# Performance work log

Measured on AMD Instinct MI355X. Metric: run time of the kernel, lower is better.

## Reference

```python
import jax, jax.numpy as jnp
import numpy as np

NUM_CODES = 1024
CODE_DIM = 256
EMA_DECAY = 0.99
COMMITMENT = 0.25
EPS = 1e-6


def setup_inputs() -> dict:
    key = jax.random.key(0)
    k1, k2 = jax.random.split(key)
    z = jax.random.normal(k1, (64, 512, CODE_DIM), dtype=jnp.float32)
    embedding = jax.random.normal(k2, (NUM_CODES, CODE_DIM), dtype=jnp.float32)
    cluster_size = jnp.zeros((NUM_CODES,), dtype=jnp.float32)
    embedding_avg = embedding.copy()
    return {"z": z, "embedding": embedding, "cluster_size": cluster_size,
            "embedding_avg": embedding_avg}


def reference(z, embedding, cluster_size, embedding_avg):
    K, D = embedding.shape
    flat = z.reshape(-1, D)                                  # [N, D]
    dist = (jnp.sum(flat * flat, axis=1, keepdims=True)
            - 2.0 * (flat @ embedding.T)
            + jnp.sum(embedding * embedding, axis=1))
    indices = jnp.argmin(dist, axis=1)                       # [N]
    z_q = embedding[indices].reshape(z.shape)

    # EMA codebook update (training branch, no-grad in original)
    counts = jax.ops.segment_sum(jnp.ones_like(indices, dtype=flat.dtype),
                                 indices, num_segments=K)    # one-hot col sums
    embed_sum = jax.ops.segment_sum(flat, indices, num_segments=K)  # [K, D]
    new_cluster_size = cluster_size * EMA_DECAY + (1.0 - EMA_DECAY) * counts
    new_embedding_avg = embedding_avg * EMA_DECAY + (1.0 - EMA_DECAY) * embed_sum
    n = jnp.sum(new_cluster_size)
    cs = (new_cluster_size + EPS) / (n + K * EPS)
    new_embedding = new_embedding_avg / cs[:, None]

    loss = COMMITMENT * jnp.mean((jax.lax.stop_gradient(z_q) - z) ** 2)
    z_q_st = z + jax.lax.stop_gradient(z_q - z)
    return (z_q_st, loss, indices, new_cluster_size, new_embedding_avg,
            new_embedding)
```

## Files before the change

kernel.cpp:

```cpp
#include <hip/hip_runtime.h>

#define N_ROWS   32768
#define KCODES   1024
#define DDIM     256
#define RPB      64
#define NBLK     512

#define O_ZQ     0
#define O_LOSS   8388608
#define O_IDX    8388609
#define O_NCS    8421377
#define O_NEA    8422401
#define O_NEMB   8684545

#define W_ESUM   0
#define W_CNT    262144
#define W_ENORM  263168
#define W_LOSSP  264192
#define W_N      265728
#define W_IDX    265792
#define W_SORT   298560
#define W_RANK   331328

typedef _Float16 half_t;
typedef __attribute__((ext_vector_type(8))) _Float16 half8;
typedef __attribute__((ext_vector_type(4))) float floatx4;

__global__ __launch_bounds__(256)
void k_prep2(const float* __restrict__ emb, float* __restrict__ enorm,
             half_t* __restrict__ Bp, float* __restrict__ zero_ws) {
    __shared__ half_t hi[16 * 256];
    __shared__ half_t lo[16 * 256];
    __shared__ float  ssum[256];
    const int ct  = blockIdx.x;
    const int tid = threadIdx.x;
    const int c16 = tid >> 4;
    const int dp  = tid & 15;

    {
        float4 z4 = {0.f, 0.f, 0.f, 0.f};
        float4* wsf4 = (float4*)zero_ws;
        int t = ct * 256 + tid;
        #pragma unroll
        for (int i = 0; i < 4; ++i) wsf4[t + i * 16384] = z4;
        if (t < 256) wsf4[65536 + t] = z4;
    }

    float ss = 0.f;
    #pragma unroll
    for (int i = 0; i < 4; ++i) {
        float4 v = *(const float4*)(emb + (size_t)(ct * 16 + c16) * DDIM + dp * 16 + i * 4);
        ss += v.x * v.x + v.y * v.y + v.z * v.z + v.w * v.w;
        #pragma unroll
        for (int q = 0; q < 4; ++q) {
            float f = (&v.x)[q];
            half_t h = (half_t)f;
            hi[c16 * 256 + dp * 16 + i * 4 + q] = h;
            lo[c16 * 256 + dp * 16 + i * 4 + q] = (half_t)(f - (float)h);
        }
    }
    ssum[tid] = ss;
    __syncthreads();
    if (tid < 16) {
        float s = 0.f;
        #pragma unroll
        for (int i = 0; i < 16; ++i) s += ssum[tid * 16 + i];
        enorm[ct * 16 + tid] = s;
    }

    const int g16 = ((ct >> 4) << 2) | ((ct >> 2) & 3);
    const int ns  = ct & 3;
    #pragma unroll
    for (int i = 0; i < 4; ++i) {
        int f    = tid + i * 256;
        int ks   = f >> 6;
        int lane = f & 63;
        int cc   = lane & 15;
        int seg  = ks >> 3;
        int ko   = (ks & 7) * 32 + (lane >> 4) * 8;
        const half_t* src = (seg == 1) ? lo : hi;
        half8 v = *(const half8*)(src + cc * 256 + ko);
        *(half8*)(Bp + (((size_t)(g16 * 16 + ks) * 4 + ns) * 64 + lane) * 8) = v;
    }
}

__global__ __launch_bounds__(512)
void k_argmin(const float* __restrict__ z, const half_t* __restrict__ Bp,
              const float* __restrict__ enorm, const float* __restrict__ embf,
              int* __restrict__ out_idx, float* __restrict__ out_idx_f,
              float* __restrict__ out_zq, float* __restrict__ lossp,
              int* __restrict__ counts_i, int* __restrict__ rank_ws) {
    __shared__ __align__(16) half_t As[RPB * 512];

    const int tid  = threadIdx.x;
    const int w    = tid >> 6;
    const int lane = tid & 63;
    const int tx   = lane & 15;
    const int quad = lane >> 4;
    const int rh   = w >> 2;
    const int cq   = w & 3;
    const int rbase = blockIdx.x * RPB;

    {
        const int arow = w * 8 + (lane >> 3);
        const int sw   = arow & 7;
        #pragma unroll
        for (int it = 0; it < 4; ++it) {
            int g = it * 8 + (lane & 7);
            const float* zp = z + (size_t)(rbase + arow) * DDIM + g * 8;
            float4 v0 = *(const float4*)zp;
            float4 v1 = *(const float4*)(zp + 4);
            half8 hi, lo;
            hi[0] = (half_t)v0.x; lo[0] = (half_t)(v0.x - (float)hi[0]);
            hi[1] = (half_t)v0.y; lo[1] = (half_t)(v0.y - (float)hi[1]);
            hi[2] = (half_t)v0.z; lo[2] = (half_t)(v0.z - (float)hi[2]);
            hi[3] = (half_t)v0.w; lo[3] = (half_t)(v0.w - (float)hi[3]);
            hi[4] = (half_t)v1.x; lo[4] = (half_t)(v1.x - (float)hi[4]);
            hi[5] = (half_t)v1.y; lo[5] = (half_t)(v1.y - (float)hi[5]);
            hi[6] = (half_t)v1.z; lo[6] = (half_t)(v1.z - (float)hi[6]);
            hi[7] = (half_t)v1.w; lo[7] = (half_t)(v1.w - (float)hi[7]);
            *(half8*)(&As[arow * 512 + ((g ^ sw)) * 8])        = hi;
            *(half8*)(&As[arow * 512 + (((32 + g) ^ sw)) * 8]) = lo;
        }
    }
    __syncthreads();

    floatx4 zero4 = {0.f, 0.f, 0.f, 0.f};
    float bd[2][4];
    int   bi[2][4];
    #pragma unroll
    for (int mt = 0; mt < 2; ++mt)
        #pragma unroll
        for (int r = 0; r < 4; ++r) { bd[mt][r] = 3.402823466e38f; bi[mt][r] = 0; }

    for (int g4 = 0; g4 < 4; ++g4) {
        const int cb = cq * 256 + g4 * 64;
        const half_t* Bg = Bp + (size_t)(cq * 4 + g4) * 32768 + (size_t)lane * 8;

        floatx4 acc[2][4];
        #pragma unroll
        for (int mt = 0; mt < 2; ++mt)
            #pragma unroll
            for (int ns = 0; ns < 4; ++ns) acc[mt][ns] = zero4;

        half8 B0[4], B1[4];
        #define LOADB(PK, BUF)                                                 \
            { const half_t* bp_ = Bg + (PK) * 2048;                            \
              _Pragma("unroll")                                                \
              for (int ns = 0; ns < 4; ++ns)                                   \
                  BUF[ns] = *(const half8*)(bp_ + ns * 512); }
        #define MFMA_BLK(AF, BUF)                                              \
            _Pragma("unroll")                                                  \
            for (int mt = 0; mt < 2; ++mt)                                     \
                _Pragma("unroll")                                              \
                for (int ns = 0; ns < 4; ++ns)                                 \
                    acc[mt][ns] = __builtin_amdgcn_mfma_f32_16x16x32_f16(      \
                        AF[mt], BUF[ns], acc[mt][ns], 0, 0, 0);

        LOADB(0, B0);
        LOADB(1, B1);

        #pragma unroll 2
        for (int s = 0; s < 8; ++s) {
            half8 a0[2], a1[2];
            #pragma unroll
            for (int mt = 0; mt < 2; ++mt) {
                int row = rh * 32 + mt * 16 + tx;
                int sw  = row & 7;
                a0[mt] = *(half8*)(&As[row * 512 + ((s * 4 + quad) ^ sw) * 8]);
                a1[mt] = *(half8*)(&As[row * 512 + ((32 + s * 4 + quad) ^ sw) * 8]);
            }
            if (s & 1) { MFMA_BLK(a0, B1) MFMA_BLK(a1, B1) LOADB(s + 2, B1); }
            else       { MFMA_BLK(a0, B0) MFMA_BLK(a1, B0) LOADB(s + 2, B0); }
        }
        #pragma unroll 2
        for (int s = 8; s < 16; ++s) {
            half8 a0[2];
            #pragma unroll
            for (int mt = 0; mt < 2; ++mt) {
                int row = rh * 32 + mt * 16 + tx;
                int sw  = row & 7;
                a0[mt] = *(half8*)(&As[row * 512 + (((s - 8) * 4 + quad) ^ sw) * 8]);
            }
            if (s & 1) { MFMA_BLK(a0, B1) if (s + 2 < 16) LOADB(s + 2, B1); }
            else       { MFMA_BLK(a0, B0) if (s + 2 < 16) LOADB(s + 2, B0); }
        }
        #undef LOADB
        #undef MFMA_BLK

        #pragma unroll
        for (int ns = 0; ns < 4; ++ns) {
            float en = enorm[cb + ns * 16 + tx];
            int   cc = cb + ns * 16 + tx;
            #pragma unroll
            for (int mt = 0; mt < 2; ++mt)
                #pragma unroll
                for (int r = 0; r < 4; ++r) {
                    float d = fmaf(-2.f, acc[mt][ns][r], en);
                    if (d < bd[mt][r]) { bd[mt][r] = d; bi[mt][r] = cc; }
                }
        }
    }

    #pragma unroll
    for (int mt = 0; mt < 2; ++mt)
        #pragma unroll
        for (int r = 0; r < 4; ++r) {
            float d = bd[mt][r];
            int   b = bi[mt][r];
            #pragma unroll
            for (int off = 8; off > 0; off >>= 1) {
                float od = __shfl_xor(d, off);
                int   ob = __shfl_xor(b, off);
                if (od < d || (od == d && ob < b)) { d = od; b = ob; }
            }
            bd[mt][r] = d; bi[mt][r] = b;
        }

    __syncthreads();
    float* sd   = (float*)As;
    int*   si   = ((int*)As) + 256;
    int*   sidx = ((int*)As) + 512;
    if (tx == 0) {
        #pragma unroll
        for (int mt = 0; mt < 2; ++mt)
            #pragma unroll
            for (int r = 0; r < 4; ++r) {
                int row = rh * 32 + mt * 16 + quad * 4 + r;
                sd[row * 4 + cq] = bd[mt][r];
                si[row * 4 + cq] = bi[mt][r];
            }
    }
    __syncthreads();
    if (tid < RPB) {
        int row = tid;
        float d = sd[row * 4];
        int   b = si[row * 4];
        #pragma unroll
        for (int ww = 1; ww < 4; ++ww) {
            float od = sd[row * 4 + ww];
            int   ob = si[row * 4 + ww];
            if (od < d || (od == d && ob < b)) { d = od; b = ob; }
        }
        sidx[row] = b;
        out_idx[rbase + row]   = b;
        out_idx_f[rbase + row] = (float)b;
        int rk = atomicAdd(&counts_i[b], 1);
        rank_ws[rbase + row] = rk;
    }
    __syncthreads();

    float l = 0.f;
    #pragma unroll
    for (int u = 0; u < 8; ++u) {
        int gi  = tid + u * 512;
        int row = gi >> 6;
        int c4  = gi & 63;
        int k   = sidx[row];
        float4 zv = *(const float4*)(z    + (size_t)(rbase + row) * DDIM + c4 * 4);
        float4 ev = *(const float4*)(embf + (size_t)k * DDIM + c4 * 4);
        float dx = ev.x - zv.x, dy = ev.y - zv.y, dz = ev.z - zv.z, dw = ev.w - zv.w;
        float4 o = { zv.x + dx, zv.y + dy, zv.z + dz, zv.w + dw };
        *(float4*)(out_zq + (size_t)(rbase + row) * DDIM + c4 * 4) = o;
        l += dx * dx + dy * dy + dz * dz + dw * dw;
    }
    #pragma unroll
    for (int off = 32; off > 0; off >>= 1) l += __shfl_down(l, off);
    __shared__ float ls[8];
    if (lane == 0) ls[w] = l;
    __syncthreads();
    if (tid == 0) {
        float s = 0.f;
        #pragma unroll
        for (int i = 0; i < 8; ++i) s += ls[i];
        lossp[blockIdx.x] = s;
    }
}

__global__ __launch_bounds__(256)
void k_scatter(const float* __restrict__ cs_in, const int* __restrict__ counts_i,
               const float* __restrict__ lossp, const int* __restrict__ idx,
               const int* __restrict__ rank_ws, int* __restrict__ rows_sorted,
               float* __restrict__ out_ncs, float* __restrict__ n_ws,
               float* __restrict__ loss_out) {
    const int tid = threadIdx.x;
    const int bid = blockIdx.x;
    __shared__ int ps[256];
    __shared__ int base_s[1024];
    __shared__ float sv[4], sl[4];

    int c[4]; int pt = 0;
    #pragma unroll
    for (int i = 0; i < 4; ++i) { c[i] = counts_i[tid * 4 + i]; pt += c[i]; }
    ps[tid] = pt;
    __syncthreads();
    for (int s = 1; s < 256; s <<= 1) {
        int v = (tid >= s) ? ps[tid - s] : 0;
        __syncthreads();
        ps[tid] += v;
        __syncthreads();
    }
    int o = ps[tid] - pt;
    float v = 0.f;
    #pragma unroll
    for (int i = 0; i < 4; ++i) {
        base_s[tid * 4 + i] = o;
        o += c[i];
        if (bid == 0) {
            float nc = cs_in[tid * 4 + i] * 0.99f + 0.01f * (float)c[i];
            out_ncs[tid * 4 + i] = nc;
            v += nc;
        }
    }
    if (bid == 0) {
        float l = lossp[tid] + lossp[tid + 256];
        #pragma unroll
        for (int off = 32; off > 0; off >>= 1) {
            v += __shfl_down(v, off);
            l += __shfl_down(l, off);
        }
        if ((tid & 63) == 0) { sv[tid >> 6] = v; sl[tid >> 6] = l; }
    }
    __syncthreads();
    if (bid == 0 && tid == 0) {
        n_ws[0]     = sv[0] + sv[1] + sv[2] + sv[3];
        loss_out[0] = 0.25f * ((sl[0] + sl[1] + sl[2] + sl[3]) / 8388608.0f);
    }
    int r = bid * 256 + tid;
    int k = idx[r];
    rows_sorted[base_s[k] + rank_ws[r]] = r;
}

__global__ __launch_bounds__(256)
void k_esum2(const float* __restrict__ z, const int* __restrict__ rows_sorted,
             const int* __restrict__ idx, float* __restrict__ esum) {
    const int tid  = threadIdx.x;
    const int w    = tid >> 6;
    const int lane = tid & 63;
    const int base = (blockIdx.x * 4 + w) * 32;

    int r = rows_sorted[base + (lane & 31)];
    int c = idx[r];
    float4 acc = {0.f, 0.f, 0.f, 0.f};
    #pragma unroll 8
    for (int j = 0; j < 32; ++j) {
        int rj = __shfl(r, j);
        int cj = __shfl(c, j);
        float4 zv = *(const float4*)(z + (size_t)rj * DDIM + lane * 4);
        acc.x += zv.x; acc.y += zv.y; acc.z += zv.z; acc.w += zv.w;
        int cn = (j < 31) ? __shfl(c, j + 1) : -1;
        if (cn != cj) {
            float* p = esum + (size_t)cj * DDIM + lane * 4;
            atomicAdd(p + 0, acc.x);
            atomicAdd(p + 1, acc.y);
            atomicAdd(p + 2, acc.z);
            atomicAdd(p + 3, acc.w);
            acc.x = 0.f; acc.y = 0.f; acc.z = 0.f; acc.w = 0.f;
        }
    }
}

__global__ __launch_bounds__(256)
void k_embed(const float* __restrict__ ea, const float* __restrict__ esum,
             const float* __restrict__ ncs, const float* __restrict__ n_ws,
             float* __restrict__ out_nea, float* __restrict__ out_nemb) {
    const int tid = threadIdx.x;
    const int kb  = blockIdx.x * 4;
    const int c   = tid >> 6;
    const int l   = tid & 63;
    size_t off = (size_t)(kb + c) * DDIM + l * 4;
    float4 av = *(const float4*)(ea   + off);
    float4 ev = *(const float4*)(esum + off);
    float4 nea = { av.x * 0.99f + 0.01f * ev.x,
                   av.y * 0.99f + 0.01f * ev.y,
                   av.z * 0.99f + 0.01f * ev.z,
                   av.w * 0.99f + 0.01f * ev.w };
    *(float4*)(out_nea + off) = nea;
    float csv = (ncs[kb + c] + 1e-6f) / (n_ws[0] + 0.001024f);
    float4 nemb = { nea.x / csv, nea.y / csv, nea.z / csv, nea.w / csv };
    *(float4*)(out_nemb + off) = nemb;
}

extern "C" void kernel_launch(void* const* d_in, const int* in_sizes, int n_in,
                              void* d_out, int out_size, void* d_ws, size_t ws_size,
                              hipStream_t stream) {
    const float* z   = (const float*)d_in[0];
    const float* emb = (const float*)d_in[1];
    const float* cs  = (const float*)d_in[2];
    const float* ea  = (const float*)d_in[3];
    float* out = (float*)d_out;
    float* ws  = (float*)d_ws;

    float* esum    = ws + W_ESUM;
    int*   cnts    = (int*)(ws + W_CNT);
    float* enorm   = ws + W_ENORM;
    float* lossp   = ws + W_LOSSP;
    float* wn      = ws + W_N;
    int*   widx    = (int*)(ws + W_IDX);
    int*   rsorted = (int*)(ws + W_SORT);
    int*   rankw   = (int*)(ws + W_RANK);

    half_t* Bp = (half_t*)(out + O_NEA + 3);

    k_prep2   <<<64, 256, 0, stream>>>(emb, enorm, Bp, ws);
    k_argmin  <<<NBLK, 512, 0, stream>>>(z, Bp, enorm, emb,
                                         widx, out + O_IDX, out + O_ZQ, lossp,
                                         cnts, rankw);
    k_scatter <<<128, 256, 0, stream>>>(cs, cnts, lossp, widx, rankw, rsorted,
                                        out + O_NCS, wn, out + O_LOSS);
    k_esum2   <<<256, 256, 0, stream>>>(z, rsorted, widx, esum);
    k_embed   <<<256, 256, 0, stream>>>(ea, esum, out + O_NCS, wn,
                                        out + O_NEA, out + O_NEMB);
}
```

Before: 179.8 us.

## Fuse scatter, esum and embed kernels into one with grid-wide spin barriers

Merges the three tail kernels into one persistent 256-block kernel. Two software grid barriers built from atomic counters in workspace replace the launch boundaries between them. Each block recomputes the cluster-size total locally, so it no longer goes through workspace. The aim is to remove two kernel launch gaps; the cost is spin-wait overhead and reliance on all 256 blocks being resident at once to avoid deadlock.

```diff
diff --git a/kernel.cpp b/kernel.cpp
--- a/kernel.cpp
+++ b/kernel.cpp
@@ -17,7 +17,7 @@
 #define W_CNT    262144
 #define W_ENORM  263168
 #define W_LOSSP  264192
-#define W_N      265728
+#define W_BAR    264704
 #define W_IDX    265792
 #define W_SORT   298560
 #define W_RANK   331328
@@ -44,6 +44,10 @@
         #pragma unroll
         for (int i = 0; i < 4; ++i) wsf4[t + i * 16384] = z4;
         if (t < 256) wsf4[65536 + t] = z4;
+        if (t == 0) {
+            int* b = (int*)(zero_ws + W_BAR);
+            b[0] = 0; b[1] = 0;
+        }
     }
 
     float ss = 0.f;
@@ -277,14 +281,29 @@
     }
 }
 
+__device__ __forceinline__ void grid_spin(int* bar, int expected) {
+    __syncthreads();
+    __threadfence();
+    if (threadIdx.x == 0) {
+        atomicAdd(bar, 1);
+        while (atomicAdd(bar, 0) < expected) __builtin_amdgcn_s_sleep(8);
+    }
+    __syncthreads();
+    __threadfence();
+}
+
 __global__ __launch_bounds__(256)
-void k_scatter(const float* __restrict__ cs_in, const int* __restrict__ counts_i,
-               const float* __restrict__ lossp, const int* __restrict__ idx,
-               const int* __restrict__ rank_ws, int* __restrict__ rows_sorted,
-               float* __restrict__ out_ncs, float* __restrict__ n_ws,
-               float* __restrict__ loss_out) {
-    const int tid = threadIdx.x;
-    const int bid = blockIdx.x;
+void k_tail3(const float* __restrict__ cs_in, const int* __restrict__ counts_i,
+             const float* __restrict__ lossp, const int* __restrict__ idx,
+             const int* __restrict__ rank_ws, const float* __restrict__ z,
+             const float* __restrict__ ea, int* __restrict__ rows_sorted,
+             float* __restrict__ esum, int* __restrict__ bar,
+             float* __restrict__ out_ncs, float* __restrict__ loss_out,
+             float* __restrict__ out_nea, float* __restrict__ out_nemb) {
+    const int tid  = threadIdx.x;
+    const int bid  = blockIdx.x;
+    const int w    = tid >> 6;
+    const int lane = tid & 63;
     __shared__ int ps[256];
     __shared__ int base_s[1024];
     __shared__ float sv[4], sl[4];
@@ -301,84 +320,76 @@
         __syncthreads();
     }
     int o = ps[tid] - pt;
-    float v = 0.f;
+    float pn = 0.f;
     #pragma unroll
     for (int i = 0; i < 4; ++i) {
         base_s[tid * 4 + i] = o;
         o += c[i];
-        if (bid == 0) {
-            float nc = cs_in[tid * 4 + i] * 0.99f + 0.01f * (float)c[i];
-            out_ncs[tid * 4 + i] = nc;
-            v += nc;
-        }
-    }
-    if (bid == 0) {
-        float l = lossp[tid] + lossp[tid + 256];
-        #pragma unroll
-        for (int off = 32; off > 0; off >>= 1) {
-            v += __shfl_down(v, off);
-            l += __shfl_down(l, off);
-        }
-        if ((tid & 63) == 0) { sv[tid >> 6] = v; sl[tid >> 6] = l; }
-    }
-    __syncthreads();
-    if (bid == 0 && tid == 0) {
-        n_ws[0]     = sv[0] + sv[1] + sv[2] + sv[3];
+        float nc = cs_in[tid * 4 + i] * 0.99f + 0.01f * (float)c[i];
+        pn += nc;
+        if (bid == 0) out_ncs[tid * 4 + i] = nc;
+    }
+    float pl = (bid == 0) ? (lossp[tid] + lossp[tid + 256]) : 0.f;
+    #pragma unroll
+    for (int off = 32; off > 0; off >>= 1) {
+        pn += __shfl_down(pn, off);
+        pl += __shfl_down(pl, off);
+    }
+    if (lane == 0) { sv[w] = pn; sl[w] = pl; }
+    __syncthreads();
+    const float nval = sv[0] + sv[1] + sv[2] + sv[3];
+    if (bid == 0 && tid == 0)
         loss_out[0] = 0.25f * ((sl[0] + sl[1] + sl[2] + sl[3]) / 8388608.0f);
-    }
-    int r = bid * 256 + tid;
-    int k = idx[r];
-    rows_sorted[base_s[k] + rank_ws[r]] = r;
-}
-
-__global__ __launch_bounds__(256)
-void k_esum2(const float* __restrict__ z, const int* __restrict__ rows_sorted,
-             const int* __restrict__ idx, float* __restrict__ esum) {
-    const int tid  = threadIdx.x;
-    const int w    = tid >> 6;
-    const int lane = tid & 63;
-    const int base = (blockIdx.x * 4 + w) * 32;
-
-    int r = rows_sorted[base + (lane & 31)];
-    int c = idx[r];
-    float4 acc = {0.f, 0.f, 0.f, 0.f};
-    #pragma unroll 8
-    for (int j = 0; j < 32; ++j) {
-        int rj = __shfl(r, j);
-        int cj = __shfl(c, j);
-        float4 zv = *(const float4*)(z + (size_t)rj * DDIM + lane * 4);
-        acc.x += zv.x; acc.y += zv.y; acc.z += zv.z; acc.w += zv.w;
-        int cn = (j < 31) ? __shfl(c, j + 1) : -1;
-        if (cn != cj) {
-            float* p = esum + (size_t)cj * DDIM + lane * 4;
-            atomicAdd(p + 0, acc.x);
-            atomicAdd(p + 1, acc.y);
-            atomicAdd(p + 2, acc.z);
-            atomicAdd(p + 3, acc.w);
-            acc.x = 0.f; acc.y = 0.f; acc.z = 0.f; acc.w = 0.f;
-        }
-    }
-}
-
-__global__ __launch_bounds__(256)
-void k_embed(const float* __restrict__ ea, const float* __restrict__ esum,
-             const float* __restrict__ ncs, const float* __restrict__ n_ws,
-             float* __restrict__ out_nea, float* __restrict__ out_nemb) {
-    const int tid = threadIdx.x;
-    const int kb  = blockIdx.x * 4;
-    const int c   = tid >> 6;
-    const int l   = tid & 63;
-    size_t off = (size_t)(kb + c) * DDIM + l * 4;
-    float4 av = *(const float4*)(ea   + off);
-    float4 ev = *(const float4*)(esum + off);
-    float4 nea = { av.x * 0.99f + 0.01f * ev.x,
-                   av.y * 0.99f + 0.01f * ev.y,
-                   av.z * 0.99f + 0.01f * ev.z,
-                   av.w * 0.99f + 0.01f * ev.w };
-    *(float4*)(out_nea + off) = nea;
-    float csv = (ncs[kb + c] + 1e-6f) / (n_ws[0] + 0.001024f);
-    float4 nemb = { nea.x / csv, nea.y / csv, nea.z / csv, nea.w / csv };
-    *(float4*)(out_nemb + off) = nemb;
+    if (tid < 128) {
+        int r = bid * 128 + tid;
+        int k = idx[r];
+        atomicExch(&rows_sorted[base_s[k] + rank_ws[r]], r);
+    }
+
+    grid_spin(&bar[0], 256);
+
+    {
+        const int base = (bid * 4 + w) * 32;
+        int r = rows_sorted[base + (lane & 31)];
+        int cc = idx[r];
+        float4 acc = {0.f, 0.f, 0.f, 0.f};
+        #pragma unroll 8
+        for (int j = 0; j < 32; ++j) {
+            int rj = __shfl(r, j);
+            int cj = __shfl(cc, j);
+            float4 zv = *(const float4*)(z + (size_t)rj * DDIM + lane * 4);
+            acc.x += zv.x; acc.y += zv.y; acc.z += zv.z; acc.w += zv.w;
+            int cn = (j < 31) ? __shfl(cc, j + 1) : -1;
+            if (cn != cj) {
+                float* p = esum + (size_t)cj * DDIM + lane * 4;
+                atomicAdd(p + 0, acc.x);
+                atomicAdd(p + 1, acc.y);
+                atomicAdd(p + 2, acc.z);
+                atomicAdd(p + 3, acc.w);
+                acc.x = 0.f; acc.y = 0.f; acc.z = 0.f; acc.w = 0.f;
+            }
+        }
+    }
+
+    grid_spin(&bar[1], 256);
+
+    {
+        const int kb = bid * 4;
+        const int cc = tid >> 6;
+        const int l  = tid & 63;
+        size_t off = (size_t)(kb + cc) * DDIM + l * 4;
+        float4 av = *(const float4*)(ea   + off);
+        float4 ev = *(const float4*)(esum + off);
+        float4 nea = { av.x * 0.99f + 0.01f * ev.x,
+                       av.y * 0.99f + 0.01f * ev.y,
+                       av.z * 0.99f + 0.01f * ev.z,
+                       av.w * 0.99f + 0.01f * ev.w };
+        *(float4*)(out_nea + off) = nea;
+        float ncv = cs_in[kb + cc] * 0.99f + 0.01f * (float)counts_i[kb + cc];
+        float csv = (ncv + 1e-6f) / (nval + 0.001024f);
+        float4 nemb = { nea.x / csv, nea.y / csv, nea.z / csv, nea.w / csv };
+        *(float4*)(out_nemb + off) = nemb;
+    }
 }
 
 extern "C" void kernel_launch(void* const* d_in, const int* in_sizes, int n_in,
@@ -395,20 +406,19 @@
     int*   cnts    = (int*)(ws + W_CNT);
     float* enorm   = ws + W_ENORM;
     float* lossp   = ws + W_LOSSP;
-    float* wn      = ws + W_N;
+    int*   bar     = (int*)(ws + W_BAR);
     int*   widx    = (int*)(ws + W_IDX);
     int*   rsorted = (int*)(ws + W_SORT);
     int*   rankw   = (int*)(ws + W_RANK);
 
     half_t* Bp = (half_t*)(out + O_NEA + 3);
 
-    k_prep2   <<<64, 256, 0, stream>>>(emb, enorm, Bp, ws);
-    k_argmin  <<<NBLK, 512, 0, stream>>>(z, Bp, enorm, emb,
-                                         widx, out + O_IDX, out + O_ZQ, lossp,
-                                         cnts, rankw);
-    k_scatter <<<128, 256, 0, stream>>>(cs, cnts, lossp, widx, rankw, rsorted,
-                                        out + O_NCS, wn, out + O_LOSS);
-    k_esum2   <<<256, 256, 0, stream>>>(z, rsorted, widx, esum);
-    k_embed   <<<256, 256, 0, stream>>>(ea, esum, out + O_NCS, wn,
-                                        out + O_NEA, out + O_NEMB);
+    k_prep2  <<<64, 256, 0, stream>>>(emb, enorm, Bp, ws);
+    k_argmin <<<NBLK, 512, 0, stream>>>(z, Bp, enorm, emb,
+                                        widx, out + O_IDX, out + O_ZQ, lossp,
+                                        cnts, rankw);
+    k_tail3  <<<256, 256, 0, stream>>>(cs, cnts, lossp, widx, rankw, z, ea,
+                                       rsorted, esum, bar,
+                                       out + O_NCS, out + O_LOSS,
+                                       out + O_NEA, out + O_NEMB);
 }
```

Measured after the change: 260.9 us. 1.45x slower.

## Fuse EMA embedding update into esum via per-code completion counters; retile argmin waves

Applied to the files above, without the earlier changes.

The separate k_embed launch is removed. Each code's new embedding_avg and embedding are now written by whichever wave finishes the last segment of that code, detected with an atomic per-code row counter. Empty codes are handled in k_scatter, which now computes n redundantly in every block. The argmin MFMA wave mapping also changes: each wave now covers all 64 rows and 32 codes per pass instead of 32 rows by 64 codes, so it loads fewer B fragments and more A fragments from LDS. The cost is a full vmcnt wait after each atomic flush plus extra atomic traffic, in exchange for one fewer kernel launch and one fewer pass over esum.

```diff
diff --git a/kernel.cpp b/kernel.cpp
--- a/kernel.cpp
+++ b/kernel.cpp
@@ -15,8 +15,9 @@
 
 #define W_ESUM   0
 #define W_CNT    262144
-#define W_ENORM  263168
-#define W_LOSSP  264192
+#define W_DONE   263168
+#define W_ENORM  264192
+#define W_LOSSP  265216
 #define W_N      265728
 #define W_IDX    265792
 #define W_SORT   298560
@@ -43,7 +44,7 @@
         int t = ct * 256 + tid;
         #pragma unroll
         for (int i = 0; i < 4; ++i) wsf4[t + i * 16384] = z4;
-        if (t < 256) wsf4[65536 + t] = z4;
+        if (t < 512) wsf4[65536 + t] = z4;
     }
 
     float ss = 0.f;
@@ -97,8 +98,6 @@
     const int lane = tid & 63;
     const int tx   = lane & 15;
     const int quad = lane >> 4;
-    const int rh   = w >> 2;
-    const int cq   = w & 3;
     const int rbase = blockIdx.x * RPB;
 
     {
@@ -126,74 +125,73 @@
     __syncthreads();
 
     floatx4 zero4 = {0.f, 0.f, 0.f, 0.f};
-    float bd[2][4];
-    int   bi[2][4];
-    #pragma unroll
-    for (int mt = 0; mt < 2; ++mt)
+    float bd[4][4];
+    int   bi[4][4];
+    #pragma unroll
+    for (int mt = 0; mt < 4; ++mt)
         #pragma unroll
         for (int r = 0; r < 4; ++r) { bd[mt][r] = 3.402823466e38f; bi[mt][r] = 0; }
 
-    for (int g4 = 0; g4 < 4; ++g4) {
-        const int cb = cq * 256 + g4 * 64;
-        const half_t* Bg = Bp + (size_t)(cq * 4 + g4) * 32768 + (size_t)lane * 8;
-
-        floatx4 acc[2][4];
-        #pragma unroll
-        for (int mt = 0; mt < 2; ++mt)
+    for (int g = 0; g < 4; ++g) {
+        const int slot = 2 * w + (g >> 1);
+        const int ns0  = (g & 1) * 2;
+        const int cb   = (slot >> 2) * 256 + (slot & 3) * 64 + ns0 * 16;
+        const half_t* Bg = Bp + (size_t)slot * 32768 + ns0 * 512 + (size_t)lane * 8;
+
+        floatx4 acc[4][2];
+        #pragma unroll
+        for (int mt = 0; mt < 4; ++mt)
             #pragma unroll
-            for (int ns = 0; ns < 4; ++ns) acc[mt][ns] = zero4;
-
-        half8 B0[4], B1[4];
+            for (int ns = 0; ns < 2; ++ns) acc[mt][ns] = zero4;
+
+        half8 B0[2], B1[2];
         #define LOADB(PK, BUF)                                                 \
             { const half_t* bp_ = Bg + (PK) * 2048;                            \
-              _Pragma("unroll")                                                \
-              for (int ns = 0; ns < 4; ++ns)                                   \
-                  BUF[ns] = *(const half8*)(bp_ + ns * 512); }
-        #define MFMA_BLK(AF, BUF)                                              \
+              BUF[0] = *(const half8*)(bp_);                                   \
+              BUF[1] = *(const half8*)(bp_ + 512); }
+        #define LDA(K8)                                                        \
             _Pragma("unroll")                                                  \
-            for (int mt = 0; mt < 2; ++mt)                                     \
+            for (int mt = 0; mt < 4; ++mt) {                                   \
+                int row = mt * 16 + tx;                                        \
+                a[mt] = *(half8*)(&As[row * 512 + (((K8) + quad) ^ (row & 7)) * 8]); \
+            }
+        #define MFMA_BLK(BUF)                                                  \
+            _Pragma("unroll")                                                  \
+            for (int mt = 0; mt < 4; ++mt)                                     \
                 _Pragma("unroll")                                              \
-                for (int ns = 0; ns < 4; ++ns)                                 \
+                for (int ns = 0; ns < 2; ++ns)                                 \
                     acc[mt][ns] = __builtin_amdgcn_mfma_f32_16x16x32_f16(      \
-                        AF[mt], BUF[ns], acc[mt][ns], 0, 0, 0);
+                        a[mt], BUF[ns], acc[mt][ns], 0, 0, 0);
 
         LOADB(0, B0);
         LOADB(1, B1);
 
         #pragma unroll 2
         for (int s = 0; s < 8; ++s) {
-            half8 a0[2], a1[2];
-            #pragma unroll
-            for (int mt = 0; mt < 2; ++mt) {
-                int row = rh * 32 + mt * 16 + tx;
-                int sw  = row & 7;
-                a0[mt] = *(half8*)(&As[row * 512 + ((s * 4 + quad) ^ sw) * 8]);
-                a1[mt] = *(half8*)(&As[row * 512 + ((32 + s * 4 + quad) ^ sw) * 8]);
-            }
-            if (s & 1) { MFMA_BLK(a0, B1) MFMA_BLK(a1, B1) LOADB(s + 2, B1); }
-            else       { MFMA_BLK(a0, B0) MFMA_BLK(a1, B0) LOADB(s + 2, B0); }
+            half8 a[4];
+            LDA(s * 4)
+            if (s & 1) { MFMA_BLK(B1) } else { MFMA_BLK(B0) }
+            LDA(32 + s * 4)
+            if (s & 1) { MFMA_BLK(B1) LOADB(s + 2, B1); }
+            else       { MFMA_BLK(B0) LOADB(s + 2, B0); }
         }
         #pragma unroll 2
         for (int s = 8; s < 16; ++s) {
-            half8 a0[2];
-            #pragma unroll
-            for (int mt = 0; mt < 2; ++mt) {
-                int row = rh * 32 + mt * 16 + tx;
-                int sw  = row & 7;
-                a0[mt] = *(half8*)(&As[row * 512 + (((s - 8) * 4 + quad) ^ sw) * 8]);
-            }
-            if (s & 1) { MFMA_BLK(a0, B1) if (s + 2 < 16) LOADB(s + 2, B1); }
-            else       { MFMA_BLK(a0, B0) if (s + 2 < 16) LOADB(s + 2, B0); }
+            half8 a[4];
+            LDA((s - 8) * 4)
+            if (s & 1) { MFMA_BLK(B1) if (s + 2 < 16) LOADB(s + 2, B1); }
+            else       { MFMA_BLK(B0) if (s + 2 < 16) LOADB(s + 2, B0); }
         }
         #undef LOADB
+        #undef LDA
         #undef MFMA_BLK
 
         #pragma unroll
-        for (int ns = 0; ns < 4; ++ns) {
+        for (int ns = 0; ns < 2; ++ns) {
             float en = enorm[cb + ns * 16 + tx];
             int   cc = cb + ns * 16 + tx;
             #pragma unroll
-            for (int mt = 0; mt < 2; ++mt)
+            for (int mt = 0; mt < 4; ++mt)
                 #pragma unroll
                 for (int r = 0; r < 4; ++r) {
                     float d = fmaf(-2.f, acc[mt][ns][r], en);
@@ -203,7 +201,7 @@
     }
 
     #pragma unroll
-    for (int mt = 0; mt < 2; ++mt)
+    for (int mt = 0; mt < 4; ++mt)
         #pragma unroll
         for (int r = 0; r < 4; ++r) {
             float d = bd[mt][r];
@@ -219,27 +217,27 @@
 
     __syncthreads();
     float* sd   = (float*)As;
-    int*   si   = ((int*)As) + 256;
-    int*   sidx = ((int*)As) + 512;
+    int*   si   = ((int*)As) + 512;
+    int*   sidx = ((int*)As) + 1024;
     if (tx == 0) {
         #pragma unroll
-        for (int mt = 0; mt < 2; ++mt)
+        for (int mt = 0; mt < 4; ++mt)
             #pragma unroll
             for (int r = 0; r < 4; ++r) {
-                int row = rh * 32 + mt * 16 + quad * 4 + r;
-                sd[row * 4 + cq] = bd[mt][r];
-                si[row * 4 + cq] = bi[mt][r];
+                int row = mt * 16 + quad * 4 + r;
+                sd[row * 8 + w] = bd[mt][r];
+                si[row * 8 + w] = bi[mt][r];
             }
     }
     __syncthreads();
     if (tid < RPB) {
         int row = tid;
-        float d = sd[row * 4];
-        int   b = si[row * 4];
-        #pragma unroll
-        for (int ww = 1; ww < 4; ++ww) {
-            float od = sd[row * 4 + ww];
-            int   ob = si[row * 4 + ww];
+        float d = sd[row * 8];
+        int   b = si[row * 8];
+        #pragma unroll
+        for (int ww = 1; ww < 8; ++ww) {
+            float od = sd[row * 8 + ww];
+            int   ob = si[row * 8 + ww];
             if (od < d || (od == d && ob < b)) { d = od; b = ob; }
         }
         sidx[row] = b;
@@ -280,11 +278,15 @@
 __global__ __launch_bounds__(256)
 void k_scatter(const float* __restrict__ cs_in, const int* __restrict__ counts_i,
                const float* __restrict__ lossp, const int* __restrict__ idx,
-               const int* __restrict__ rank_ws, int* __restrict__ rows_sorted,
+               const int* __restrict__ rank_ws, const float* __restrict__ ea,
+               int* __restrict__ rows_sorted,
                float* __restrict__ out_ncs, float* __restrict__ n_ws,
-               float* __restrict__ loss_out) {
+               float* __restrict__ loss_out,
+               float* __restrict__ out_nea, float* __restrict__ out_nemb) {
     const int tid = threadIdx.x;
     const int bid = blockIdx.x;
+    const int w    = tid >> 6;
+    const int lane = tid & 63;
     __shared__ int ps[256];
     __shared__ int base_s[1024];
     __shared__ float sv[4], sl[4];
@@ -301,53 +303,74 @@
         __syncthreads();
     }
     int o = ps[tid] - pt;
-    float v = 0.f;
+    float pn = 0.f;
     #pragma unroll
     for (int i = 0; i < 4; ++i) {
         base_s[tid * 4 + i] = o;
         o += c[i];
-        if (bid == 0) {
-            float nc = cs_in[tid * 4 + i] * 0.99f + 0.01f * (float)c[i];
-            out_ncs[tid * 4 + i] = nc;
-            v += nc;
-        }
-    }
-    if (bid == 0) {
-        float l = lossp[tid] + lossp[tid + 256];
-        #pragma unroll
-        for (int off = 32; off > 0; off >>= 1) {
-            v += __shfl_down(v, off);
-            l += __shfl_down(l, off);
-        }
-        if ((tid & 63) == 0) { sv[tid >> 6] = v; sl[tid >> 6] = l; }
-    }
-    __syncthreads();
+        float nc = cs_in[tid * 4 + i] * 0.99f + 0.01f * (float)c[i];
+        pn += nc;
+        if (bid == 0) out_ncs[tid * 4 + i] = nc;
+    }
+    float pl = (bid == 0) ? (lossp[tid] + lossp[tid + 256]) : 0.f;
+    #pragma unroll
+    for (int off = 32; off > 0; off >>= 1) {
+        pn += __shfl_down(pn, off);
+        pl += __shfl_down(pl, off);
+    }
+    if (lane == 0) { sv[w] = pn; sl[w] = pl; }
+    __syncthreads();
+    const float nval = sv[0] + sv[1] + sv[2] + sv[3];
     if (bid == 0 && tid == 0) {
-        n_ws[0]     = sv[0] + sv[1] + sv[2] + sv[3];
+        n_ws[0]     = nval;
         loss_out[0] = 0.25f * ((sl[0] + sl[1] + sl[2] + sl[3]) / 8388608.0f);
     }
-    int r = bid * 256 + tid;
-    int k = idx[r];
-    rows_sorted[base_s[k] + rank_ws[r]] = r;
+    {
+        int r = bid * 256 + tid;
+        int k = idx[r];
+        rows_sorted[base_s[k] + rank_ws[r]] = r;
+    }
+    #pragma unroll
+    for (int pass = 0; pass < 2; ++pass) {
+        int k = bid * 8 + pass * 4 + (tid >> 6);
+        if (counts_i[k] == 0) {
+            int l2 = tid & 63;
+            size_t off = (size_t)k * DDIM + l2 * 4;
+            float4 av = *(const float4*)(ea + off);
+            float4 nea = { av.x * 0.99f, av.y * 0.99f, av.z * 0.99f, av.w * 0.99f };
+            *(float4*)(out_nea + off) = nea;
+            float ncv = cs_in[k] * 0.99f;
+            float csv = (ncv + 1e-6f) / (nval + 0.001024f);
+            float4 nemb = { nea.x / csv, nea.y / csv, nea.z / csv, nea.w / csv };
+            *(float4*)(out_nemb + off) = nemb;
+        }
+    }
 }
 
 __global__ __launch_bounds__(256)
-void k_esum2(const float* __restrict__ z, const int* __restrict__ rows_sorted,
-             const int* __restrict__ idx, float* __restrict__ esum) {
+void k_esum3(const float* __restrict__ z, const int* __restrict__ rows_sorted,
+             const int* __restrict__ idx, const int* __restrict__ counts_i,
+             const float* __restrict__ cs_in, const float* __restrict__ n_ws,
+             const float* __restrict__ ea, float* __restrict__ esum,
+             int* __restrict__ done,
+             float* __restrict__ out_nea, float* __restrict__ out_nemb) {
     const int tid  = threadIdx.x;
     const int w    = tid >> 6;
     const int lane = tid & 63;
     const int base = (blockIdx.x * 4 + w) * 32;
+    const float nval = n_ws[0];
 
     int r = rows_sorted[base + (lane & 31)];
     int c = idx[r];
     float4 acc = {0.f, 0.f, 0.f, 0.f};
-    #pragma unroll 8
+    int rlen = 0;
+    #pragma unroll 4
     for (int j = 0; j < 32; ++j) {
         int rj = __shfl(r, j);
         int cj = __shfl(c, j);
         float4 zv = *(const float4*)(z + (size_t)rj * DDIM + lane * 4);
         acc.x += zv.x; acc.y += zv.y; acc.z += zv.z; acc.w += zv.w;
+        rlen++;
         int cn = (j < 31) ? __shfl(c, j + 1) : -1;
         if (cn != cj) {
             float* p = esum + (size_t)cj * DDIM + lane * 4;
@@ -355,30 +378,36 @@
             atomicAdd(p + 1, acc.y);
             atomicAdd(p + 2, acc.z);
             atomicAdd(p + 3, acc.w);
+            asm volatile("s_waitcnt vmcnt(0)" ::: "memory");
+            int last = 0;
+            if (lane == 0) {
+                int old = atomicAdd(&done[cj], rlen);
+                last = (old + rlen == counts_i[cj]) ? 1 : 0;
+            }
+            last = __shfl(last, 0);
+            if (last) {
+                float* q = esum + (size_t)cj * DDIM + lane * 4;
+                float4 ev;
+                ev.x = atomicAdd(q + 0, 0.f);
+                ev.y = atomicAdd(q + 1, 0.f);
+                ev.z = atomicAdd(q + 2, 0.f);
+                ev.w = atomicAdd(q + 3, 0.f);
+                size_t off = (size_t)cj * DDIM + lane * 4;
+                float4 av = *(const float4*)(ea + off);
+                float4 nea = { av.x * 0.99f + 0.01f * ev.x,
+                               av.y * 0.99f + 0.01f * ev.y,
+                               av.z * 0.99f + 0.01f * ev.z,
+                               av.w * 0.99f + 0.01f * ev.w };
+                *(float4*)(out_nea + off) = nea;
+                float ncv = cs_in[cj] * 0.99f + 0.01f * (float)counts_i[cj];
+                float csv = (ncv + 1e-6f) / (nval + 0.001024f);
+                float4 nemb = { nea.x / csv, nea.y / csv, nea.z / csv, nea.w / csv };
+                *(float4*)(out_nemb + off) = nemb;
+            }
             acc.x = 0.f; acc.y = 0.f; acc.z = 0.f; acc.w = 0.f;
-        }
-    }
-}
-
-__global__ __launch_bounds__(256)
-void k_embed(const float* __restrict__ ea, const float* __restrict__ esum,
-             const float* __restrict__ ncs, const float* __restrict__ n_ws,
-             float* __restrict__ out_nea, float* __restrict__ out_nemb) {
-    const int tid = threadIdx.x;
-    const int kb  = blockIdx.x * 4;
-    const int c   = tid >> 6;
-    const int l   = tid & 63;
-    size_t off = (size_t)(kb + c) * DDIM + l * 4;
-    float4 av = *(const float4*)(ea   + off);
-    float4 ev = *(const float4*)(esum + off);
-    float4 nea = { av.x * 0.99f + 0.01f * ev.x,
-                   av.y * 0.99f + 0.01f * ev.y,
-                   av.z * 0.99f + 0.01f * ev.z,
-                   av.w * 0.99f + 0.01f * ev.w };
-    *(float4*)(out_nea + off) = nea;
-    float csv = (ncs[kb + c] + 1e-6f) / (n_ws[0] + 0.001024f);
-    float4 nemb = { nea.x / csv, nea.y / csv, nea.z / csv, nea.w / csv };
-    *(float4*)(out_nemb + off) = nemb;
+            rlen = 0;
+        }
+    }
 }
 
 extern "C" void kernel_launch(void* const* d_in, const int* in_sizes, int n_in,
@@ -393,6 +422,7 @@
 
     float* esum    = ws + W_ESUM;
     int*   cnts    = (int*)(ws + W_CNT);
+    int*   done    = (int*)(ws + W_DONE);
     float* enorm   = ws + W_ENORM;
     float* lossp   = ws + W_LOSSP;
     float* wn      = ws + W_N;
@@ -406,9 +436,9 @@
     k_argmin  <<<NBLK, 512, 0, stream>>>(z, Bp, enorm, emb,
                                          widx, out + O_IDX, out + O_ZQ, lossp,
                                          cnts, rankw);
-    k_scatter <<<128, 256, 0, stream>>>(cs, cnts, lossp, widx, rankw, rsorted,
-                                        out + O_NCS, wn, out + O_LOSS);
-    k_esum2   <<<256, 256, 0, stream>>>(z, rsorted, widx, esum);
-    k_embed   <<<256, 256, 0, stream>>>(ea, esum, out + O_NCS, wn,
+    k_scatter <<<128, 256, 0, stream>>>(cs, cnts, lossp, widx, rankw, ea,
+                                        rsorted, out + O_NCS, wn, out + O_LOSS,
                                         out + O_NEA, out + O_NEMB);
+    k_esum3   <<<256, 256, 0, stream>>>(z, rsorted, widx, cnts, cs, wn, ea,
+                                        esum, done, out + O_NEA, out + O_NEMB);
 }
```

After: 184.3 us. 1.03x slower.

## Halve rows per block and split codebook across all eight waves

Applied to the files above, without the earlier changes.

Each argmin block now handles 32 rows instead of 64, so twice as many blocks launch. All eight waves share the same 32 rows, and each wave scans 128 codes instead of 256. The cross-wave reduction now combines eight candidates per row, and the finalize kernel sums 1024 loss partials. This is meant to improve occupancy and load balance across CUs, at the cost of doubling total codebook reads from L2 and giving each B fragment less reuse.

```diff
diff --git a/kernel.cpp b/kernel.cpp
--- a/kernel.cpp
+++ b/kernel.cpp
@@ -3,8 +3,8 @@
 #define N_ROWS   32768
 #define KCODES   1024
 #define DDIM     256
-#define RPB      64
-#define NBLK     512
+#define RPB      32
+#define NBLK     1024
 
 #define O_ZQ     0
 #define O_LOSS   8388608
@@ -97,31 +97,28 @@
     const int lane = tid & 63;
     const int tx   = lane & 15;
     const int quad = lane >> 4;
-    const int rh   = w >> 2;
-    const int cq   = w & 3;
     const int rbase = blockIdx.x * RPB;
 
-    {
-        const int arow = w * 8 + (lane >> 3);
-        const int sw   = arow & 7;
-        #pragma unroll
-        for (int it = 0; it < 4; ++it) {
-            int g = it * 8 + (lane & 7);
-            const float* zp = z + (size_t)(rbase + arow) * DDIM + g * 8;
-            float4 v0 = *(const float4*)zp;
-            float4 v1 = *(const float4*)(zp + 4);
-            half8 hi, lo;
-            hi[0] = (half_t)v0.x; lo[0] = (half_t)(v0.x - (float)hi[0]);
-            hi[1] = (half_t)v0.y; lo[1] = (half_t)(v0.y - (float)hi[1]);
-            hi[2] = (half_t)v0.z; lo[2] = (half_t)(v0.z - (float)hi[2]);
-            hi[3] = (half_t)v0.w; lo[3] = (half_t)(v0.w - (float)hi[3]);
-            hi[4] = (half_t)v1.x; lo[4] = (half_t)(v1.x - (float)hi[4]);
-            hi[5] = (half_t)v1.y; lo[5] = (half_t)(v1.y - (float)hi[5]);
-            hi[6] = (half_t)v1.z; lo[6] = (half_t)(v1.z - (float)hi[6]);
-            hi[7] = (half_t)v1.w; lo[7] = (half_t)(v1.w - (float)hi[7]);
-            *(half8*)(&As[arow * 512 + ((g ^ sw)) * 8])        = hi;
-            *(half8*)(&As[arow * 512 + (((32 + g) ^ sw)) * 8]) = lo;
-        }
+    #pragma unroll
+    for (int it = 0; it < 2; ++it) {
+        int f   = tid + it * 512;
+        int row = f >> 5;
+        int g   = f & 31;
+        const float* zp = z + (size_t)(rbase + row) * DDIM + g * 8;
+        float4 v0 = *(const float4*)zp;
+        float4 v1 = *(const float4*)(zp + 4);
+        half8 hi, lo;
+        hi[0] = (half_t)v0.x; lo[0] = (half_t)(v0.x - (float)hi[0]);
+        hi[1] = (half_t)v0.y; lo[1] = (half_t)(v0.y - (float)hi[1]);
+        hi[2] = (half_t)v0.z; lo[2] = (half_t)(v0.z - (float)hi[2]);
+        hi[3] = (half_t)v0.w; lo[3] = (half_t)(v0.w - (float)hi[3]);
+        hi[4] = (half_t)v1.x; lo[4] = (half_t)(v1.x - (float)hi[4]);
+        hi[5] = (half_t)v1.y; lo[5] = (half_t)(v1.y - (float)hi[5]);
+        hi[6] = (half_t)v1.z; lo[6] = (half_t)(v1.z - (float)hi[6]);
+        hi[7] = (half_t)v1.w; lo[7] = (half_t)(v1.w - (float)hi[7]);
+        int sw = row & 7;
+        *(half8*)(&As[row * 512 + ((g ^ sw)) * 8])        = hi;
+        *(half8*)(&As[row * 512 + (((32 + g) ^ sw)) * 8]) = lo;
     }
     __syncthreads();
 
@@ -133,9 +130,10 @@
         #pragma unroll
         for (int r = 0; r < 4; ++r) { bd[mt][r] = 3.402823466e38f; bi[mt][r] = 0; }
 
-    for (int g4 = 0; g4 < 4; ++g4) {
-        const int cb = cq * 256 + g4 * 64;
-        const half_t* Bg = Bp + (size_t)(cq * 4 + g4) * 32768 + (size_t)lane * 8;
+    for (int gs = 0; gs < 2; ++gs) {
+        const int slot = 2 * w + gs;
+        const int cb   = slot * 64;
+        const half_t* Bg = Bp + (size_t)slot * 32768 + (size_t)lane * 8;
 
         floatx4 acc[2][4];
         #pragma unroll
@@ -165,7 +163,7 @@
             half8 a0[2], a1[2];
             #pragma unroll
             for (int mt = 0; mt < 2; ++mt) {
-                int row = rh * 32 + mt * 16 + tx;
+                int row = mt * 16 + tx;
                 int sw  = row & 7;
                 a0[mt] = *(half8*)(&As[row * 512 + ((s * 4 + quad) ^ sw) * 8]);
                 a1[mt] = *(half8*)(&As[row * 512 + ((32 + s * 4 + quad) ^ sw) * 8]);
@@ -178,7 +176,7 @@
             half8 a0[2];
             #pragma unroll
             for (int mt = 0; mt < 2; ++mt) {
-                int row = rh * 32 + mt * 16 + tx;
+                int row = mt * 16 + tx;
                 int sw  = row & 7;
                 a0[mt] = *(half8*)(&As[row * 512 + (((s - 8) * 4 + quad) ^ sw) * 8]);
             }
@@ -226,20 +224,20 @@
         for (int mt = 0; mt < 2; ++mt)
             #pragma unroll
             for (int r = 0; r < 4; ++r) {
-                int row = rh * 32 + mt * 16 + quad * 4 + r;
-                sd[row * 4 + cq] = bd[mt][r];
-                si[row * 4 + cq] = bi[mt][r];
+                int row = mt * 16 + quad * 4 + r;
+                sd[row * 8 + w] = bd[mt][r];
+                si[row * 8 + w] = bi[mt][r];
             }
     }
     __syncthreads();
     if (tid < RPB) {
         int row = tid;
-        float d = sd[row * 4];
-        int   b = si[row * 4];
-        #pragma unroll
-        for (int ww = 1; ww < 4; ++ww) {
-            float od = sd[row * 4 + ww];
-            int   ob = si[row * 4 + ww];
+        float d = sd[row * 8];
+        int   b = si[row * 8];
+        #pragma unroll
+        for (int ww = 1; ww < 8; ++ww) {
+            float od = sd[row * 8 + ww];
+            int   ob = si[row * 8 + ww];
             if (od < d || (od == d && ob < b)) { d = od; b = ob; }
         }
         sidx[row] = b;
@@ -252,7 +250,7 @@
 
     float l = 0.f;
     #pragma unroll
-    for (int u = 0; u < 8; ++u) {
+    for (int u = 0; u < 4; ++u) {
         int gi  = tid + u * 512;
         int row = gi >> 6;
         int c4  = gi & 63;
@@ -313,7 +311,7 @@
         }
     }
     if (bid == 0) {
-        float l = lossp[tid] + lossp[tid + 256];
+        float l = lossp[tid] + lossp[tid + 256] + lossp[tid + 512] + lossp[tid + 768];
         #pragma unroll
         for (int off = 32; off > 0; off >>= 1) {
             v += __shfl_down(v, off);
```

New measurement: 178.3 us. No clear change (-0.8%).
